# Kernel optimization log

Hardware: AMD Instinct MI355X
Metric: run time of the kernel (lower is better)

The kernel has to match this reference:

```python
import jax, jax.numpy as jnp
import numpy as np
import math

PHI = (1.0 + math.sqrt(5.0)) / 2.0
TWO_PI = 2.0 * math.pi
LUT_N = 4096  # hard-coded LUT size in the torch module
_ANG = jnp.arange(LUT_N, dtype=jnp.float32) * (TWO_PI / LUT_N)
COS_TABLE = jnp.cos(_ANG)


def _lut_cos(theta):
    # quantize angle to LUT_N bins over [0, 2*pi) and look up cos
    frac = theta * (1.0 / TWO_PI)
    frac = frac - jnp.floor(frac)
    idx = jnp.clip(jnp.floor(frac * LUT_N).astype(jnp.int32), 0, LUT_N - 1)
    return COS_TABLE[idx]


def setup_inputs() -> dict:
    key = jax.random.key(0)
    k1, k2, k3 = jax.random.split(key, 3)
    B, S, D = 2, 8192, 64
    states_real = jax.random.normal(k1, (B, S, D), dtype=jnp.float32)
    states_imag = jax.random.normal(k2, (B, S, D), dtype=jnp.float32)
    positions = jnp.arange(S, dtype=jnp.float32)
    w_q = jax.random.normal(k3, (D,), dtype=jnp.float32) * 0.02
    b_q = jnp.zeros((D,), dtype=jnp.float32)
    alpha = jnp.asarray(0.1, dtype=jnp.float32)
    return {"states_real": states_real, "states_imag": states_imag,
            "positions": positions, "w_q": w_q, "b_q": b_q, "alpha": alpha}


def reference(states_real, states_imag, positions, w_q, b_q, alpha):
    B, S, D = states_real.shape
    scale = math.sqrt(2 * D)
    wl_q = 1.0 + jnp.abs(w_q)                      # (D,)
    t_phi = (positions * PHI)[None, :, None]       # (1,S,1)
    theta_r = states_real / wl_q + b_q + t_phi     # (B,S,D)
    theta_i = states_imag / wl_q + b_q + t_phi
    Q = jnp.concatenate([_lut_cos(theta_r), _lut_cos(theta_i)], axis=-1)  # (B,S,2D)
    K = jnp.concatenate([states_real, states_imag], axis=-1)              # (B,S,2D)
    scores = jnp.einsum('bqd,bkd->bqk', Q, K) / scale                     # (B,S,S)
    causal = jnp.triu(jnp.ones((S, S), dtype=bool), k=1)
    scores = jnp.where(causal[None], -jnp.inf, scores)
    scores = scores.at[:, 0, 0].set(0.0)
    attn = jax.nn.softmax(scores, axis=-1)
    retrieved = jnp.einsum('bqk,bkd->bqd', attn, K)                       # (B,S,2D)
    a = jax.nn.sigmoid(alpha)

    def step(ema, r_t):
        ema = a * r_t + (1.0 - a) * ema
        return ema, ema

    ema0 = jnp.zeros((B, 2 * D), dtype=states_real.dtype)
    _, ema_states = jax.lax.scan(step, ema0, jnp.swapaxes(retrieved, 0, 1))  # (S,B,2D)
    ema_states = jnp.swapaxes(ema_states, 0, 1)                              # (B,S,2D)
    return ema_states[..., :D] + ema_states[..., D:]
```

## Files before the change

### kernel.cpp

```cpp
#include <hip/hip_runtime.h>
#include <hip/hip_bf16.h>

typedef short short8 __attribute__((ext_vector_type(8)));
typedef float f32x16 __attribute__((ext_vector_type(16)));
typedef int   int2v  __attribute__((ext_vector_type(2)));

#define S_LEN 8192
#define NB 2
#define HD 128
#define KTILE 64
#define NQT 64
#define NPAIR 32
#define NCK 12

__device__ __forceinline__ unsigned short f2bf(float f){
  union { float f; unsigned u; } v; v.f = f;
  unsigned r = v.u + 0x7fff + ((v.u>>16)&1);
  return (unsigned short)(r>>16);
}

__device__ __forceinline__ float lutcos(float theta){
  float fr = theta * 0.15915494309189535f;
  fr = fr - floorf(fr);
  int idx = (int)floorf(fr * 4096.0f);
  idx = idx < 0 ? 0 : (idx > 4095 ? 4095 : idx);
  return __cosf((float)idx * 0.0015339807878856412f);
}

__device__ __forceinline__ unsigned cvtpk_bf16(float lo, float hi){
  unsigned r;
  asm("v_cvt_pk_bf16_f32 %0, %1, %2" : "=v"(r) : "v"(lo), "v"(hi));
  return r;
}

__global__ __launch_bounds__(256)
void precomp_kernel(const float* __restrict__ SR, const float* __restrict__ SI,
                    const float* __restrict__ POS, const float* __restrict__ WQ,
                    const float* __restrict__ BQ,
                    short* __restrict__ Qbf, short* __restrict__ Kbf)
{
  int id  = blockIdx.x*256 + threadIdx.x;
  int row = id >> 4;
  int d0  = (id & 15) * 8;
  int s   = row & (S_LEN-1);
  const float* src = (d0 < 64) ? (SR + (long)row*64 + d0)
                               : (SI + (long)row*64 + (d0-64));
  float4 x0 = *(const float4*)src;
  float4 x1 = *(const float4*)(src+4);
  float xs[8] = {x0.x,x0.y,x0.z,x0.w,x1.x,x1.y,x1.z,x1.w};
  float tphi = POS[s] * 1.618033988749895f;
  int dm = d0 & 63;
  short8 kq, qq;
  #pragma unroll
  for (int j=0;j<8;j++){
    kq[j] = (short)f2bf(xs[j]);
    float wl = 1.0f + fabsf(WQ[dm+j]);
    float th = xs[j]/wl + BQ[dm+j] + tphi;
    qq[j] = (short)f2bf(lutcos(th));
  }
  *(short8*)(Kbf + (long)row*HD + d0) = kq;
  *(short8*)(Qbf + (long)row*HD + d0) = qq;
}

__global__ __launch_bounds__(256,3)
void attn_pair(const short* __restrict__ Qbf, const short* __restrict__ Kbf,
               float* __restrict__ OW, float* __restrict__ LW)
{
  const int pr = blockIdx.x;
  const int ck = blockIdx.y;
  const int b  = blockIdx.z;
  const int qa = pr, qb = NQT-1-pr;
  const int na = 2*(qa+1);
  int lo = ck*10 + min(ck,10);
  int hi = lo + 10 + (ck<10 ? 1 : 0);

  const int tid  = threadIdx.x;
  const int lane = tid & 63;
  const int wv   = tid >> 6;
  const int l31  = lane & 31;
  const int h5   = lane >> 5;

  __shared__ short ldsK[KTILE*HD];
  __shared__ short ldsV[HD*KTILE];

  const float iscale = 0.08838834764831845f;
  const long rowbase = (long)b*S_LEN;

  #pragma unroll 1
  for (int sg=0; sg<2; ++sg){
    int slo = sg ? max(lo,na) : lo;
    int shi = sg ? hi : min(hi,na);
    if (slo >= shi) continue;
    const int qt = sg ? qb : qa;
    const int t0 = slo - (sg ? na : 0);
    const int t1 = shi - (sg ? na : 0);
    const int qg = qt*128 + wv*32 + l31;

    short8 qf[8];
    #pragma unroll
    for (int ds=0; ds<8; ds++)
      qf[ds] = *(const short8*)(Qbf + (rowbase+qg)*HD + ds*16 + h5*8);

    f32x16 oacc[4];
    #pragma unroll
    for (int dt=0;dt<4;dt++) oacc[dt] = (f32x16)0.0f;
    float lsum = 0.0f;

    #pragma unroll 1
    for (int kt=t0; kt<t1; ++kt){
      const int kvbase = kt*KTILE;
      const short* kb = Kbf + (rowbase + kvbase)*HD;
      __syncthreads();

      #pragma unroll
      for (int it=0; it<4; it++){
        int id  = tid + it*256;
        int row = id >> 4;
        int c8  = (id & 15)*8;
        short8 h = *(const short8*)(kb + row*HD + c8);
        *(short8*)&ldsK[(row*HD + c8) ^ ((row&15)<<3)] = h;
      }
      #pragma unroll
      for (int it=0; it<2; it++){
        int id  = tid + it*256;
        int kv2 = id & 31;
        int d0  = (id >> 5)*8;
        const short* r0 = kb + (2*kv2)*HD + d0;
        short8 a = *(const short8*)r0;
        short8 c = *(const short8*)(r0 + HD);
        #pragma unroll
        for (int j=0;j<8;j++){
          unsigned pj = ((unsigned)(unsigned short)a[j]) | (((unsigned)(unsigned short)c[j])<<16);
          int d = d0+j;
          *(unsigned*)&ldsV[(d*KTILE + 2*kv2) ^ ((d&7)<<3)] = pj;
        }
      }
      __syncthreads();

      #pragma unroll 1
      for (int nb=0; nb<2; ++nb){
        f32x16 sacc = (f32x16)0.0f;
        __builtin_amdgcn_s_setprio(1);
        #pragma unroll
        for (int ds=0; ds<8; ds++){
          int row = nb*32 + l31;
          short8 kf = *(short8*)&ldsK[(row*HD + ds*16 + h5*8) ^ ((row&15)<<3)];
          sacc = __builtin_amdgcn_mfma_f32_32x32x16_bf16(kf, qf[ds], sacc, 0,0,0);
        }
        __builtin_amdgcn_s_setprio(0);

        unsigned w[8];
        #pragma unroll
        for (int g=0; g<2; ++g){
          float p[8];
          #pragma unroll
          for (int rr=0; rr<8; rr++){
            int r = g*8 + rr;
            int kvg = kvbase + nb*32 + (r&3) + 8*(r>>2) + 4*h5;
            float s = sacc[r]*iscale;
            float pe = (kvg <= qg) ? __expf(s) : 0.0f;
            lsum += pe;
            p[rr] = pe;
          }
          unsigned x0 = cvtpk_bf16(p[0],p[1]);
          unsigned x1 = cvtpk_bf16(p[2],p[3]);
          unsigned y0 = cvtpk_bf16(p[4],p[5]);
          unsigned y1 = cvtpk_bf16(p[6],p[7]);
          int2v r0 = __builtin_amdgcn_permlane32_swap((int)x0, (int)y0, false, false);
          int2v r1 = __builtin_amdgcn_permlane32_swap((int)x1, (int)y1, false, false);
          w[g*4+0]=(unsigned)r0[0]; w[g*4+1]=(unsigned)r1[0];
          w[g*4+2]=(unsigned)r0[1]; w[g*4+3]=(unsigned)r1[1];
        }
        union { unsigned u[4]; short8 s; } pa0, pa1;
        pa0.u[0]=w[0]; pa0.u[1]=w[1]; pa0.u[2]=w[2]; pa0.u[3]=w[3];
        pa1.u[0]=w[4]; pa1.u[1]=w[5]; pa1.u[2]=w[6]; pa1.u[3]=w[7];

        __builtin_amdgcn_s_setprio(1);
        #pragma unroll
        for (int dt=0; dt<4; dt++){
          int row = dt*32 + l31;
          int cb  = nb*32 + h5*8;
          short8 v0 = *(short8*)&ldsV[(row*KTILE + cb     ) ^ ((row&7)<<3)];
          short8 v1 = *(short8*)&ldsV[(row*KTILE + cb + 16) ^ ((row&7)<<3)];
          oacc[dt] = __builtin_amdgcn_mfma_f32_32x32x16_bf16(pa0.s, v0, oacc[dt], 0,0,0);
          oacc[dt] = __builtin_amdgcn_mfma_f32_32x32x16_bf16(pa1.s, v1, oacc[dt], 0,0,0);
        }
        __builtin_amdgcn_s_setprio(0);
      }
    }

    float tot = lsum + __shfl_xor(lsum, 32);
    if (lane < 32) atomicAdd(&LW[rowbase + qg], tot);
    #pragma unroll
    for (int dt=0; dt<4; dt++){
      #pragma unroll
      for (int r=0; r<16; r++){
        int qrow = qt*128 + wv*32 + (r&3) + 8*(r>>2) + 4*h5;
        atomicAdd(&OW[(rowbase + qrow)*HD + dt*32 + l31], oacc[dt][r]);
      }
    }
  }
}

__global__ __launch_bounds__(64)
void ema_kernel(const float* __restrict__ OW, const float* __restrict__ LW,
                const float* __restrict__ ALPHA, float* __restrict__ out)
{
  int d = threadIdx.x;
  int p = blockIdx.x;
  int b = blockIdx.y;
  float a  = 1.0f/(1.0f + __expf(-ALPHA[0]));
  float na = 1.0f - a;
  int t0 = p*32;
  int tw = t0 - ((p>0)?32:0);
  float ema = 0.0f;
  #pragma unroll 8
  for (int t=tw; t<t0+32; ++t){
    long base = (long)b*S_LEN + t;
    float l = LW[base];
    float o = OW[base*HD + d] + OW[base*HD + d + 64];
    float u = o / l;
    ema = a*u + na*ema;
    if (t>=t0) out[base*64 + d] = ema;
  }
}

extern "C" void kernel_launch(void* const* d_in, const int* in_sizes, int n_in,
                              void* d_out, int out_size, void* d_ws, size_t ws_size,
                              hipStream_t stream)
{
  const float* SR    = (const float*)d_in[0];
  const float* SI    = (const float*)d_in[1];
  const float* POS   = (const float*)d_in[2];
  const float* WQ    = (const float*)d_in[3];
  const float* BQv   = (const float*)d_in[4];
  const float* ALPHA = (const float*)d_in[5];

  float* OW  = (float*)d_ws;
  float* LW  = OW + (size_t)NB*S_LEN*HD;
  short* Qbf = (short*)(LW + (size_t)NB*S_LEN);
  short* Kbf = Qbf + (size_t)NB*S_LEN*HD;
  size_t zbytes = ((size_t)NB*S_LEN*HD + (size_t)NB*S_LEN)*sizeof(float);
  hipMemsetAsync(d_ws, 0, zbytes, stream);

  precomp_kernel<<<dim3(NB*S_LEN*16/256), 256, 0, stream>>>(SR, SI, POS, WQ, BQv, Qbf, Kbf);
  attn_pair<<<dim3(NPAIR, NCK, NB), 256, 0, stream>>>(Qbf, Kbf, OW, LW);
  ema_kernel<<<dim3(S_LEN/32, NB), 64, 0, stream>>>(OW, LW, ALPHA, (float*)d_out);
}
```

Measured before the change: 171.2 us.

## Split causal mask to diagonal tiles, fold scale into Q, parallelize EMA

Folds the 1/sqrt(2D) score scale into Q during precompute, so the attention kernel no longer multiplies every score. Splits the KV loop into unmasked tiles and masked diagonal tiles via a template, so the causal compare runs only on the tiles that need it. The EMA kernel now uses smaller 16-step chunks with a 16-step warmup, prefetches the loads into registers and uses a reciprocal instruction instead of a divide. The shorter EMA warmup and the rounding of Q to bf16 after scaling both change numerics slightly.

After: 162.9 us. 4.8% less time.

```diff
diff --git a/kernel.cpp b/kernel.cpp
--- a/kernel.cpp
+++ b/kernel.cpp
@@ -12,6 +12,8 @@
 #define NQT 64
 #define NPAIR 32
 #define NCK 12
+#define ECH 16
+#define EWM 16
 
 __device__ __forceinline__ unsigned short f2bf(float f){
   union { float f; unsigned u; } v; v.f = f;
@@ -49,6 +51,7 @@
   float4 x1 = *(const float4*)(src+4);
   float xs[8] = {x0.x,x0.y,x0.z,x0.w,x1.x,x1.y,x1.z,x1.w};
   float tphi = POS[s] * 1.618033988749895f;
+  const float iscale = 0.08838834764831845f;
   int dm = d0 & 63;
   short8 kq, qq;
   #pragma unroll
@@ -56,10 +59,99 @@
     kq[j] = (short)f2bf(xs[j]);
     float wl = 1.0f + fabsf(WQ[dm+j]);
     float th = xs[j]/wl + BQ[dm+j] + tphi;
-    qq[j] = (short)f2bf(lutcos(th));
+    qq[j] = (short)f2bf(iscale * lutcos(th));
   }
   *(short8*)(Kbf + (long)row*HD + d0) = kq;
   *(short8*)(Qbf + (long)row*HD + d0) = qq;
+}
+
+template<bool MASKED>
+__device__ __forceinline__ void attn_tile(
+    const short* __restrict__ kb,
+    int kvbase, int qg,
+    short* ldsK, short* ldsV,
+    const short8 (&qf)[8], f32x16 (&oacc)[4], float& lsum,
+    int tid, int l31, int h5)
+{
+  __syncthreads();
+  #pragma unroll
+  for (int it=0; it<4; it++){
+    int id  = tid + it*256;
+    int row = id >> 4;
+    int c8  = (id & 15)*8;
+    short8 h = *(const short8*)(kb + row*HD + c8);
+    *(short8*)&ldsK[(row*HD + c8) ^ ((row&15)<<3)] = h;
+  }
+  #pragma unroll
+  for (int it=0; it<2; it++){
+    int id  = tid + it*256;
+    int kv2 = id & 31;
+    int d0  = (id >> 5)*8;
+    const short* r0 = kb + (2*kv2)*HD + d0;
+    short8 a = *(const short8*)r0;
+    short8 c = *(const short8*)(r0 + HD);
+    #pragma unroll
+    for (int j=0;j<8;j++){
+      unsigned pj = ((unsigned)(unsigned short)a[j]) | (((unsigned)(unsigned short)c[j])<<16);
+      int d = d0+j;
+      *(unsigned*)&ldsV[(d*KTILE + 2*kv2) ^ ((d&7)<<3)] = pj;
+    }
+  }
+  __syncthreads();
+
+  #pragma unroll 1
+  for (int nb=0; nb<2; ++nb){
+    f32x16 sacc = (f32x16)0.0f;
+    __builtin_amdgcn_s_setprio(1);
+    #pragma unroll
+    for (int ds=0; ds<8; ds++){
+      int row = nb*32 + l31;
+      short8 kf = *(short8*)&ldsK[(row*HD + ds*16 + h5*8) ^ ((row&15)<<3)];
+      sacc = __builtin_amdgcn_mfma_f32_32x32x16_bf16(kf, qf[ds], sacc, 0,0,0);
+    }
+    __builtin_amdgcn_s_setprio(0);
+
+    unsigned w[8];
+    #pragma unroll
+    for (int g=0; g<2; ++g){
+      float p[8];
+      #pragma unroll
+      for (int rr=0; rr<8; rr++){
+        int r = g*8 + rr;
+        float s = sacc[r];
+        if (MASKED){
+          int kvg = kvbase + nb*32 + (r&3) + 8*(r>>2) + 4*h5;
+          s = (kvg <= qg) ? s : -1e30f;
+        }
+        float pe = __expf(s);
+        lsum += pe;
+        p[rr] = pe;
+      }
+      unsigned x0 = cvtpk_bf16(p[0],p[1]);
+      unsigned x1 = cvtpk_bf16(p[2],p[3]);
+      unsigned y0 = cvtpk_bf16(p[4],p[5]);
+      unsigned y1 = cvtpk_bf16(p[6],p[7]);
+      int2v r0 = __builtin_amdgcn_permlane32_swap((int)x0, (int)y0, false, false);
+      int2v r1 = __builtin_amdgcn_permlane32_swap((int)x1, (int)y1, false, false);
+      w[g*4+0]=(unsigned)r0[0]; w[g*4+1]=(unsigned)r1[0];
+      w[g*4+2]=(unsigned)r0[1]; w[g*4+3]=(unsigned)r1[1];
+    }
+    union { unsigned u[4]; short8 s; } pa0, pa1;
+    pa0.u[0]=w[0]; pa0.u[1]=w[1]; pa0.u[2]=w[2]; pa0.u[3]=w[3];
+    pa1.u[0]=w[4]; pa1.u[1]=w[5]; pa1.u[2]=w[6]; pa1.u[3]=w[7];
+
+    __builtin_amdgcn_s_setprio(1);
+    #pragma unroll
+    for (int dt=0; dt<4; dt++){
+      int row = dt*32 + l31;
+      int cb  = nb*32 + h5*8;
+      short8 v0 = *(short8*)&ldsV[(row*KTILE + cb     ) ^ ((row&7)<<3)];
+      short8 v1 = *(short8*)&ldsV[(row*KTILE + cb + 16) ^ ((row&7)<<3)];
+      oacc[dt] = __builtin_amdgcn_mfma_f32_32x32x16_bf16(pa0.s, v0, oacc[dt], 0,0,0);
+      oacc[dt] = __builtin_amdgcn_mfma_f32_32x32x16_bf16(pa1.s, v1, oacc[dt], 0,0,0);
+    }
+    __builtin_amdgcn_s_setprio(0);
+  }
 }
 
 __global__ __launch_bounds__(256,3)
@@ -83,7 +175,6 @@
   __shared__ short ldsK[KTILE*HD];
   __shared__ short ldsV[HD*KTILE];
 
-  const float iscale = 0.08838834764831845f;
   const long rowbase = (long)b*S_LEN;
 
   #pragma unroll 1
@@ -106,88 +197,16 @@
     for (int dt=0;dt<4;dt++) oacc[dt] = (f32x16)0.0f;
     float lsum = 0.0f;
 
+    const int tmask = 2*qt;
+    const int u_end = min(t1, tmask);
     #pragma unroll 1
-    for (int kt=t0; kt<t1; ++kt){
-      const int kvbase = kt*KTILE;
-      const short* kb = Kbf + (rowbase + kvbase)*HD;
-      __syncthreads();
-
-      #pragma unroll
-      for (int it=0; it<4; it++){
-        int id  = tid + it*256;
-        int row = id >> 4;
-        int c8  = (id & 15)*8;
-        short8 h = *(const short8*)(kb + row*HD + c8);
-        *(short8*)&ldsK[(row*HD + c8) ^ ((row&15)<<3)] = h;
-      }
-      #pragma unroll
-      for (int it=0; it<2; it++){
-        int id  = tid + it*256;
-        int kv2 = id & 31;
-        int d0  = (id >> 5)*8;
-        const short* r0 = kb + (2*kv2)*HD + d0;
-        short8 a = *(const short8*)r0;
-        short8 c = *(const short8*)(r0 + HD);
-        #pragma unroll
-        for (int j=0;j<8;j++){
-          unsigned pj = ((unsigned)(unsigned short)a[j]) | (((unsigned)(unsigned short)c[j])<<16);
-          int d = d0+j;
-          *(unsigned*)&ldsV[(d*KTILE + 2*kv2) ^ ((d&7)<<3)] = pj;
-        }
-      }
-      __syncthreads();
-
-      #pragma unroll 1
-      for (int nb=0; nb<2; ++nb){
-        f32x16 sacc = (f32x16)0.0f;
-        __builtin_amdgcn_s_setprio(1);
-        #pragma unroll
-        for (int ds=0; ds<8; ds++){
-          int row = nb*32 + l31;
-          short8 kf = *(short8*)&ldsK[(row*HD + ds*16 + h5*8) ^ ((row&15)<<3)];
-          sacc = __builtin_amdgcn_mfma_f32_32x32x16_bf16(kf, qf[ds], sacc, 0,0,0);
-        }
-        __builtin_amdgcn_s_setprio(0);
-
-        unsigned w[8];
-        #pragma unroll
-        for (int g=0; g<2; ++g){
-          float p[8];
-          #pragma unroll
-          for (int rr=0; rr<8; rr++){
-            int r = g*8 + rr;
-            int kvg = kvbase + nb*32 + (r&3) + 8*(r>>2) + 4*h5;
-            float s = sacc[r]*iscale;
-            float pe = (kvg <= qg) ? __expf(s) : 0.0f;
-            lsum += pe;
-            p[rr] = pe;
-          }
-          unsigned x0 = cvtpk_bf16(p[0],p[1]);
-          unsigned x1 = cvtpk_bf16(p[2],p[3]);
-          unsigned y0 = cvtpk_bf16(p[4],p[5]);
-          unsigned y1 = cvtpk_bf16(p[6],p[7]);
-          int2v r0 = __builtin_amdgcn_permlane32_swap((int)x0, (int)y0, false, false);
-          int2v r1 = __builtin_amdgcn_permlane32_swap((int)x1, (int)y1, false, false);
-          w[g*4+0]=(unsigned)r0[0]; w[g*4+1]=(unsigned)r1[0];
-          w[g*4+2]=(unsigned)r0[1]; w[g*4+3]=(unsigned)r1[1];
-        }
-        union { unsigned u[4]; short8 s; } pa0, pa1;
-        pa0.u[0]=w[0]; pa0.u[1]=w[1]; pa0.u[2]=w[2]; pa0.u[3]=w[3];
-        pa1.u[0]=w[4]; pa1.u[1]=w[5]; pa1.u[2]=w[6]; pa1.u[3]=w[7];
-
-        __builtin_amdgcn_s_setprio(1);
-        #pragma unroll
-        for (int dt=0; dt<4; dt++){
-          int row = dt*32 + l31;
-          int cb  = nb*32 + h5*8;
-          short8 v0 = *(short8*)&ldsV[(row*KTILE + cb     ) ^ ((row&7)<<3)];
-          short8 v1 = *(short8*)&ldsV[(row*KTILE + cb + 16) ^ ((row&7)<<3)];
-          oacc[dt] = __builtin_amdgcn_mfma_f32_32x32x16_bf16(pa0.s, v0, oacc[dt], 0,0,0);
-          oacc[dt] = __builtin_amdgcn_mfma_f32_32x32x16_bf16(pa1.s, v1, oacc[dt], 0,0,0);
-        }
-        __builtin_amdgcn_s_setprio(0);
-      }
-    }
+    for (int kt=t0; kt<u_end; ++kt)
+      attn_tile<false>(Kbf + (rowbase + kt*KTILE)*HD, kt*KTILE, qg,
+                       ldsK, ldsV, qf, oacc, lsum, tid, l31, h5);
+    #pragma unroll 1
+    for (int kt=max(t0,tmask); kt<t1; ++kt)
+      attn_tile<true >(Kbf + (rowbase + kt*KTILE)*HD, kt*KTILE, qg,
+                       ldsK, ldsV, qf, oacc, lsum, tid, l31, h5);
 
     float tot = lsum + __shfl_xor(lsum, 32);
     if (lane < 32) atomicAdd(&LW[rowbase + qg], tot);
@@ -211,17 +230,27 @@
   int b = blockIdx.y;
   float a  = 1.0f/(1.0f + __expf(-ALPHA[0]));
   float na = 1.0f - a;
-  int t0 = p*32;
-  int tw = t0 - ((p>0)?32:0);
+  int t0 = p*ECH;
+  int tw = (p>0) ? (t0-EWM) : 0;
+  int n  = t0+ECH - tw;
+  long base0 = (long)b*S_LEN + tw;
+  float ov[32], lv[32];
+  #pragma unroll
+  for (int i=0;i<32;i++){
+    if (i<n){
+      ov[i] = OW[(base0+i)*HD + d] + OW[(base0+i)*HD + d + 64];
+      lv[i] = LW[base0+i];
+    }
+  }
   float ema = 0.0f;
-  #pragma unroll 8
-  for (int t=tw; t<t0+32; ++t){
-    long base = (long)b*S_LEN + t;
-    float l = LW[base];
-    float o = OW[base*HD + d] + OW[base*HD + d + 64];
-    float u = o / l;
-    ema = a*u + na*ema;
-    if (t>=t0) out[base*64 + d] = ema;
+  #pragma unroll
+  for (int i=0;i<32;i++){
+    if (i<n){
+      float u = ov[i] * __builtin_amdgcn_rcpf(lv[i]);
+      ema = a*u + na*ema;
+      int t = tw+i;
+      if (t>=t0) out[((long)b*S_LEN + t)*64 + d] = ema;
+    }
   }
 }
 
@@ -245,5 +274,5 @@
 
   precomp_kernel<<<dim3(NB*S_LEN*16/256), 256, 0, stream>>>(SR, SI, POS, WQ, BQv, Qbf, Kbf);
   attn_pair<<<dim3(NPAIR, NCK, NB), 256, 0, stream>>>(Qbf, Kbf, OW, LW);
-  ema_kernel<<<dim3(S_LEN/32, NB), 64, 0, stream>>>(OW, LW, ALPHA, (float*)d_out);
-}
+  ema_kernel<<<dim3(S_LEN/ECH, NB), 64, 0, stream>>>(OW, LW, ALPHA, (float*)d_out);
+}
```
